# Optimization experiments

Measured on AMD Instinct MI355X. Metric: run time of the kernel, lower is better.

## Reference

```python
import jax, jax.numpy as jnp
import numpy as np

NUM_HEADS = 12


def setup_inputs() -> dict:
    key = jax.random.key(0)
    ks = jax.random.split(key, 6)
    C = 768
    hd = C // NUM_HEADS  # 64
    H = W = 32
    x = jax.random.normal(ks[0], (4, H, W, C), dtype=jnp.float32)
    # Linear weights stored as (in, out) so y = x @ W (+ b)
    Wqkv = jax.random.normal(ks[1], (C, 3 * C), dtype=jnp.float32) * 0.02
    Wproj = jax.random.normal(ks[2], (C, C), dtype=jnp.float32) * 0.02
    bproj = jax.random.normal(ks[3], (C,), dtype=jnp.float32) * 0.02
    rel_pos_h = jax.random.normal(ks[4], (2 * H - 1, hd), dtype=jnp.float32) * 0.02
    rel_pos_w = jax.random.normal(ks[5], (2 * W - 1, hd), dtype=jnp.float32) * 0.02
    return {"x": x, "Wqkv": Wqkv, "Wproj": Wproj, "bproj": bproj,
            "rel_pos_h": rel_pos_h, "rel_pos_w": rel_pos_w}


def _get_rel_pos(size: int, rel_pos: jnp.ndarray) -> jnp.ndarray:
    # q_size == k_size == size; table already has 2*size-1 entries -> no interpolation
    coords = jnp.arange(size)[:, None] - jnp.arange(size)[None, :] + (size - 1)
    return rel_pos[coords]  # (size, size, head_dim)


def reference(x, Wqkv, Wproj, bproj, rel_pos_h, rel_pos_w):
    B, H, W, C = x.shape
    hn = NUM_HEADS
    hd = C // hn
    scale = hd ** (-0.5)
    S = H * W

    qkv = x @ Wqkv                                   # (B,H,W,3C)
    qkv = qkv.reshape(B, S, 3, hn, hd)
    qkv = jnp.transpose(qkv, (2, 0, 3, 1, 4)).reshape(3, B * hn, S, hd)
    q, k, v = qkv[0], qkv[1], qkv[2]                 # each (B*hn, S, hd)

    # decomposed relative position bias
    Rh = _get_rel_pos(H, rel_pos_h)                  # (H,H,hd)
    Rw = _get_rel_pos(W, rel_pos_w)                  # (W,W,hd)
    r_q = q.reshape(B * hn, H, W, hd)
    rel_h = jnp.einsum('bhwc,hkc->bhwk', r_q, Rh)    # (B*hn,H,W,H)
    rel_w = jnp.einsum('bhwc,wkc->bhwk', r_q, Rw)    # (B*hn,H,W,W)
    bias = rel_h[..., :, None] + rel_w[..., None, :] # (B*hn,H,W,H,W)
    bias = bias.reshape(B * hn, S, S)

    scores = scale * jnp.einsum('bqc,bkc->bqk', q, k) + bias
    attn = jax.nn.softmax(scores, axis=-1)
    out = jnp.einsum('bqk,bkc->bqc', attn, v)        # (B*hn,S,hd)

    out = out.reshape(B, hn, H, W, hd)
    out = jnp.transpose(out, (0, 2, 3, 1, 4)).reshape(B, H, W, C)
    return out @ Wproj + bproj
```

## Files before the change

### kernel.cpp

```cpp
#include <hip/hip_runtime.h>
#include <stddef.h>

typedef __bf16 bf16x8 __attribute__((ext_vector_type(8)));
typedef __bf16 bf16x4 __attribute__((ext_vector_type(4)));
typedef float  f32x4  __attribute__((ext_vector_type(4)));

#define MFMA16(a, b, c) __builtin_amdgcn_mfma_f32_16x16x32_bf16((a), (b), (c), 0, 0, 0)

__device__ __forceinline__ void gload_lds16(const void* gsrc, void* ldst) {
    __builtin_amdgcn_global_load_lds(
        (__attribute__((address_space(1))) void*)gsrc,
        (__attribute__((address_space(3))) void*)ldst,
        16, 0, 0);
}

__global__ void prep_kernel(const float* __restrict__ x, __bf16* __restrict__ xbf,
                            const float* __restrict__ Wqkv, __bf16* __restrict__ WqkvT,
                            const float* __restrict__ Wproj, __bf16* __restrict__ WprojT) {
    __shared__ float tile[32][33];
    const int bx = blockIdx.x, tid = threadIdx.x;
    if (bx < 3072) {
        int i = bx * 256 + tid;
        float4 v = ((const float4*)x)[i];
        bf16x4 o = {(__bf16)v.x, (__bf16)v.y, (__bf16)v.z, (__bf16)v.w};
        ((bf16x4*)xbf)[i] = o;
        return;
    }
    const float* in; __bf16* out; int R, C, c0, r0;
    if (bx < 4800) { int bb = bx - 3072; in = Wqkv;  out = WqkvT;  R = 768; C = 2304;
                     c0 = (bb % 72) * 32; r0 = (bb / 72) * 32; }
    else           { int bb = bx - 4800; in = Wproj; out = WprojT; R = 768; C = 768;
                     c0 = (bb % 24) * 32; r0 = (bb / 24) * 32; }
    const int tx = tid & 31, ty = tid >> 5;
#pragma unroll
    for (int i = 0; i < 32; i += 8)
        tile[ty + i][tx] = in[(size_t)(r0 + ty + i) * C + c0 + tx];
    __syncthreads();
#pragma unroll
    for (int i = 0; i < 32; i += 8)
        out[(size_t)(c0 + ty + i) * R + r0 + tx] = (__bf16)tile[tx][ty + i];
}

__device__ __forceinline__ void gemm_core_bk64(
    const __bf16* __restrict__ A, const __bf16* __restrict__ Bt, int K,
    int m0, int n0, __bf16* aT, __bf16* bT, f32x4 acc[4][4]) {
    const int tid  = threadIdx.x;
    const int wid  = tid >> 6, lane = tid & 63;
    const int quad = lane >> 4, l16 = lane & 15;
    const int wm = (wid >> 1) * 64, wn = (wid & 1) * 64;
    const int r_in = lane >> 3;
    const int cswz = ((lane & 7) ^ r_in) * 8;
    const __bf16* gA = A  + (size_t)(m0 + wid * 8 + r_in) * K + cswz;
    const __bf16* gB = Bt + (size_t)(n0 + wid * 8 + r_in) * K + cswz;
    const int sA = (l16 & 7);
    for (int k0 = 0; k0 < K; k0 += 64) {
        __syncthreads();
#pragma unroll
        for (int j = 0; j < 4; j++) {
            gload_lds16(gA + (size_t)(j * 32) * K + k0, aT + (j * 32 + wid * 8) * 64);
            gload_lds16(gB + (size_t)(j * 32) * K + k0, bT + (j * 32 + wid * 8) * 64);
        }
        __syncthreads();
#pragma unroll
        for (int kh = 0; kh < 2; kh++) {
            bf16x8 af[4], bfr[4];
#pragma unroll
            for (int t = 0; t < 4; t++) {
                const int slot = ((kh * 4 + quad) ^ sA) << 3;
                af[t]  = *(const bf16x8*)(aT + (wm + t * 16 + l16) * 64 + slot);
                bfr[t] = *(const bf16x8*)(bT + (wn + t * 16 + l16) * 64 + slot);
            }
#pragma unroll
            for (int rt = 0; rt < 4; rt++)
#pragma unroll
                for (int ct = 0; ct < 4; ct++)
                    acc[rt][ct] = MFMA16(af[rt], bfr[ct], acc[rt][ct]);
        }
    }
}

__global__ __launch_bounds__(256, 3)
void gemm_qkv_kernel(const __bf16* __restrict__ A, const __bf16* __restrict__ Bt,
                     __bf16* __restrict__ qb, __bf16* __restrict__ kb,
                     __bf16* __restrict__ vtb) {
    __shared__ __bf16 aT[8192], bT[8192];
    f32x4 acc[4][4];
#pragma unroll
    for (int i = 0; i < 4; i++)
#pragma unroll
        for (int j = 0; j < 4; j++) { f32x4 z = {0.f, 0.f, 0.f, 0.f}; acc[i][j] = z; }
    const int m0 = blockIdx.x * 128, n0 = blockIdx.y * 128;
    gemm_core_bk64(A, Bt, 768, m0, n0, aT, bT, acc);
    const int tid = threadIdx.x, wid = tid >> 6, lane = tid & 63;
    const int quad = lane >> 4, l16 = lane & 15;
    const int wm = (wid >> 1) * 64, wn = (wid & 1) * 64;
#pragma unroll
    for (int rt = 0; rt < 4; rt++)
#pragma unroll
        for (int ct = 0; ct < 4; ct++) {
            const int ng = n0 + wn + ct * 16 + l16;
            const int which = ng / 768;
            const int rem = ng - which * 768;
            const int hh = rem >> 6, d = rem & 63;
#pragma unroll
            for (int r = 0; r < 4; r++) {
                const int mg = m0 + wm + rt * 16 + quad * 4 + r;
                const int b = mg >> 10, s = mg & 1023;
                const int bh = b * 12 + hh;
                __bf16 bv = (__bf16)acc[rt][ct][r];
                if (which == 0)      qb[((size_t)bh * 1024 + s) * 64 + d] = bv;
                else if (which == 1) kb[((size_t)bh * 1024 + s) * 64 + d] = bv;
                else                 vtb[((size_t)bh * 64 + d) * 1024 + s] = bv;
            }
        }
}

__global__ __launch_bounds__(256, 3)
void gemm_proj_kernel(const __bf16* __restrict__ A, const __bf16* __restrict__ Bt,
                      const float* __restrict__ bias, float* __restrict__ out) {
    __shared__ __bf16 aT[8192], bT[8192];
    f32x4 acc[4][4];
#pragma unroll
    for (int i = 0; i < 4; i++)
#pragma unroll
        for (int j = 0; j < 4; j++) { f32x4 z = {0.f, 0.f, 0.f, 0.f}; acc[i][j] = z; }
    const int m0 = blockIdx.x * 128, n0 = blockIdx.y * 128;
    gemm_core_bk64(A, Bt, 768, m0, n0, aT, bT, acc);
    const int tid = threadIdx.x, wid = tid >> 6, lane = tid & 63;
    const int quad = lane >> 4, l16 = lane & 15;
    const int wm = (wid >> 1) * 64, wn = (wid & 1) * 64;
#pragma unroll
    for (int rt = 0; rt < 4; rt++)
#pragma unroll
        for (int ct = 0; ct < 4; ct++) {
            const int ng = n0 + wn + ct * 16 + l16;
            const float bb = bias[ng];
#pragma unroll
            for (int r = 0; r < 4; r++) {
                const int mg = m0 + wm + rt * 16 + quad * 4 + r;
                out[(size_t)mg * 768 + ng] = acc[rt][ct][r] + bb;
            }
        }
}

__global__ __launch_bounds__(128, 2)
void attn_kernel(const __bf16* __restrict__ q, const __bf16* __restrict__ kk,
                 const __bf16* __restrict__ vt, const float* __restrict__ rph,
                 const float* __restrict__ rpw, __bf16* __restrict__ aout) {
    __shared__ __bf16 kv[2][8192];
    __shared__ __bf16 pbuf[2][32 * 72];
    __shared__ float  relh[64][33];
    const int tid = threadIdx.x, wid = tid >> 6, lane = tid & 63;
    const int quad = lane >> 4, l16 = lane & 15;
    const int bh = blockIdx.x, qt = blockIdx.y;
    const int b = bh / 12, hh = bh - b * 12;
    const int q0 = qt * 64;
    const int w0 = wid * 32;
    const int h = qt * 2 + wid;

    bf16x8 aq[2][2];
#pragma unroll
    for (int rt = 0; rt < 2; rt++) {
        const __bf16* qp = q + ((size_t)bh * 1024 + q0 + w0 + rt * 16 + l16) * 64;
        aq[rt][0] = *(const bf16x8*)(qp + quad * 8);
        aq[rt][1] = *(const bf16x8*)(qp + 32 + quad * 8);
    }

    float* Dw = ((float*)kv) + wid * 2048;
#pragma unroll
    for (int ct = 0; ct < 4; ct++) {
        int j = ct * 16 + l16; if (j > 62) j = 62;
        const float* tb = rpw + (size_t)j * 64;
        float4 t0 = *(const float4*)(tb + quad * 8);
        float4 t1 = *(const float4*)(tb + quad * 8 + 4);
        float4 t2 = *(const float4*)(tb + 32 + quad * 8);
        float4 t3 = *(const float4*)(tb + 32 + quad * 8 + 4);
        bf16x8 b0 = {(__bf16)t0.x, (__bf16)t0.y, (__bf16)t0.z, (__bf16)t0.w,
                     (__bf16)t1.x, (__bf16)t1.y, (__bf16)t1.z, (__bf16)t1.w};
        bf16x8 b1 = {(__bf16)t2.x, (__bf16)t2.y, (__bf16)t2.z, (__bf16)t2.w,
                     (__bf16)t3.x, (__bf16)t3.y, (__bf16)t3.z, (__bf16)t3.w};
#pragma unroll
        for (int rt = 0; rt < 2; rt++) {
            f32x4 z = {0.f, 0.f, 0.f, 0.f};
            z = MFMA16(aq[rt][0], b0, z);
            z = MFMA16(aq[rt][1], b1, z);
#pragma unroll
            for (int i = 0; i < 4; i++)
                Dw[(rt * 16 + quad * 4 + i) * 64 + ct * 16 + l16] = z[i];
        }
    }
#pragma unroll
    for (int ct = 0; ct < 2; ct++) {
        const int tr = h - (ct * 16 + l16) + 31;
        const float* tb = rph + (size_t)tr * 64;
        float4 t0 = *(const float4*)(tb + quad * 8);
        float4 t1 = *(const float4*)(tb + quad * 8 + 4);
        float4 t2 = *(const float4*)(tb + 32 + quad * 8);
        float4 t3 = *(const float4*)(tb + 32 + quad * 8 + 4);
        bf16x8 b0 = {(__bf16)t0.x, (__bf16)t0.y, (__bf16)t0.z, (__bf16)t0.w,
                     (__bf16)t1.x, (__bf16)t1.y, (__bf16)t1.z, (__bf16)t1.w};
        bf16x8 b1 = {(__bf16)t2.x, (__bf16)t2.y, (__bf16)t2.z, (__bf16)t2.w,
                     (__bf16)t3.x, (__bf16)t3.y, (__bf16)t3.z, (__bf16)t3.w};
#pragma unroll
        for (int rt = 0; rt < 2; rt++) {
            f32x4 z = {0.f, 0.f, 0.f, 0.f};
            z = MFMA16(aq[rt][0], b0, z);
            z = MFMA16(aq[rt][1], b1, z);
#pragma unroll
            for (int i = 0; i < 4; i++)
                relh[w0 + rt * 16 + quad * 4 + i][ct * 16 + l16] = z[i];
        }
    }
    float bw[2][2][4];
#pragma unroll
    for (int rt = 0; rt < 2; rt++)
#pragma unroll
        for (int r = 0; r < 4; r++) {
            const int row = rt * 16 + quad * 4 + r;
            bw[rt][0][r] = Dw[row * 64 + row - l16 + 31];
            bw[rt][1][r] = Dw[row * 64 + row + 15 - l16];
        }
    __syncthreads();

    float l_run[2][4];
    f32x4 o_acc[2][4];
#pragma unroll
    for (int rt = 0; rt < 2; rt++)
#pragma unroll
        for (int r = 0; r < 4; r++) l_run[rt][r] = 0.f;
#pragma unroll
    for (int rt = 0; rt < 2; rt++)
#pragma unroll
        for (int t = 0; t < 4; t++) { f32x4 z = {0.f, 0.f, 0.f, 0.f}; o_acc[rt][t] = z; }

    const __bf16* kg0 = kk + (size_t)bh * 65536;
    const __bf16* vg0 = vt + (size_t)bh * 65536;
    const int cbase = wid * 4;
    const int srow = lane >> 3;
    const int scol = ((lane & 7) ^ srow) * 8;
    const int swz0 = ((quad ^ (l16 & 7)) << 3);
    const int swz1 = (((quad | 4) ^ (l16 & 7)) << 3);
    __bf16* pw = pbuf[wid];

    auto stage = [&](int buf, int kt) {
        const __bf16* kg = kg0 + kt * 4096;
        const __bf16* vg = vg0 + kt * 64;
        __bf16* kb_ = &kv[buf][0];
        __bf16* vb_ = &kv[buf][4096];
#pragma unroll
        for (int j = 0; j < 4; j++) {
            const int c = cbase + j;
            gload_lds16(kg + (c * 8 + srow) * 64 + scol, kb_ + c * 512);
            gload_lds16(vg + (size_t)(c * 8 + srow) * 1024 + scol, vb_ + c * 512);
        }
    };

    stage(0, 0);
    for (int kt = 0; kt < 16; kt++) {
        const int cur = kt & 1;
        __syncthreads();
        if (kt < 15) stage(1 - cur, kt + 1);
        const __bf16* kbuf = &kv[cur][0];
        const __bf16* vbuf = &kv[cur][4096];

        bf16x8 bk[4][2];
#pragma unroll
        for (int ct = 0; ct < 4; ct++) {
            const int key = ct * 16 + l16;
            bk[ct][0] = *(const bf16x8*)(kbuf + key * 64 + swz0);
            bk[ct][1] = *(const bf16x8*)(kbuf + key * 64 + swz1);
        }

#pragma unroll
        for (int rt = 0; rt < 2; rt++) {
            f32x4 sacc[4];
#pragma unroll
            for (int ct = 0; ct < 4; ct++) {
                f32x4 z = {0.f, 0.f, 0.f, 0.f};
                z = MFMA16(aq[rt][0], bk[ct][0], z);
                z = MFMA16(aq[rt][1], bk[ct][1], z);
                sacc[ct] = z;
            }
            float bh0[4], bh1[4];
#pragma unroll
            for (int r = 0; r < 4; r++) {
                bh0[r] = relh[w0 + rt * 16 + quad * 4 + r][kt * 2];
                bh1[r] = relh[w0 + rt * 16 + quad * 4 + r][kt * 2 + 1];
            }
#pragma unroll
            for (int ct = 0; ct < 4; ct++)
#pragma unroll
                for (int r = 0; r < 4; r++) {
                    float sv = fmaf(sacc[ct][r], 0.125f,
                                    (ct < 2 ? bh0[r] : bh1[r]) +
                                    ((ct & 1) ? bw[rt][1][r] : bw[rt][0][r]));
                    float p = __expf(sv);
                    l_run[rt][r] += p;
                    pw[(rt * 16 + quad * 4 + r) * 72 + ct * 16 + l16] = (__bf16)p;
                }
        }

#pragma unroll
        for (int nt = 0; nt < 4; nt++) {
            const int d = nt * 16 + l16;
            bf16x8 bv0 = *(const bf16x8*)(vbuf + d * 64 + swz0);
            bf16x8 bv1 = *(const bf16x8*)(vbuf + d * 64 + swz1);
#pragma unroll
            for (int rt = 0; rt < 2; rt++) {
                bf16x8 ap0 = *(const bf16x8*)(pw + (rt * 16 + l16) * 72 + quad * 8);
                bf16x8 ap1 = *(const bf16x8*)(pw + (rt * 16 + l16) * 72 + 32 + quad * 8);
                o_acc[rt][nt] = MFMA16(ap0, bv0, o_acc[rt][nt]);
                o_acc[rt][nt] = MFMA16(ap1, bv1, o_acc[rt][nt]);
            }
        }
    }

#pragma unroll
    for (int rt = 0; rt < 2; rt++)
#pragma unroll
        for (int r = 0; r < 4; r++) {
            float s = l_run[rt][r];
            s += __shfl_xor(s, 1);
            s += __shfl_xor(s, 2);
            s += __shfl_xor(s, 4);
            s += __shfl_xor(s, 8);
            l_run[rt][r] = 1.f / s;
        }
#pragma unroll
    for (int rt = 0; rt < 2; rt++) {
        const int srow_o = q0 + w0 + rt * 16 + quad * 4;
#pragma unroll
        for (int nt = 0; nt < 4; nt++)
#pragma unroll
            for (int r = 0; r < 4; r++) {
                float v = o_acc[rt][nt][r] * l_run[rt][r];
                aout[((size_t)b * 1024 + srow_o + r) * 768 + hh * 64 + nt * 16 + l16] = (__bf16)v;
            }
    }
}

extern "C" void kernel_launch(void* const* d_in, const int* in_sizes, int n_in,
                              void* d_out, int out_size, void* d_ws, size_t ws_size,
                              hipStream_t stream) {
    const float* x     = (const float*)d_in[0];
    const float* Wqkv  = (const float*)d_in[1];
    const float* Wproj = (const float*)d_in[2];
    const float* bproj = (const float*)d_in[3];
    const float* rph   = (const float*)d_in[4];
    const float* rpw   = (const float*)d_in[5];
    float* out = (float*)d_out;
    char* ws = (char*)d_ws;

    __bf16* xbf    = (__bf16*)(ws);
    __bf16* WqkvT  = (__bf16*)(ws + 6291456);
    __bf16* WprojT = (__bf16*)(ws + 9830400);
    __bf16* qb     = (__bf16*)(ws + 11010048);
    __bf16* kb     = (__bf16*)(ws + 17301504);
    __bf16* vtb    = (__bf16*)(ws + 23592960);
    __bf16* aob    = (__bf16*)(ws + 29884416);

    prep_kernel<<<dim3(5376), dim3(256), 0, stream>>>(x, xbf, Wqkv, WqkvT, Wproj, WprojT);
    gemm_qkv_kernel<<<dim3(32, 18), dim3(256), 0, stream>>>(xbf, WqkvT, qb, kb, vtb);
    attn_kernel<<<dim3(48, 16), dim3(128), 0, stream>>>(qb, kb, vtb, rph, rpw, aob);
    gemm_proj_kernel<<<dim3(32, 6), dim3(256), 0, stream>>>(aob, WprojT, bproj, out);
}
```

Before: 154.4 us.

## Split attention query tile across four waves of 16 rows each

```diff
diff --git a/kernel.cpp b/kernel.cpp
--- a/kernel.cpp
+++ b/kernel.cpp
@@ -143,30 +143,26 @@
         }
 }
 
-__global__ __launch_bounds__(128, 2)
+__global__ __launch_bounds__(256, 3)
 void attn_kernel(const __bf16* __restrict__ q, const __bf16* __restrict__ kk,
                  const __bf16* __restrict__ vt, const float* __restrict__ rph,
                  const float* __restrict__ rpw, __bf16* __restrict__ aout) {
     __shared__ __bf16 kv[2][8192];
-    __shared__ __bf16 pbuf[2][32 * 72];
+    __shared__ __bf16 pbuf[4][16 * 72];
     __shared__ float  relh[64][33];
     const int tid = threadIdx.x, wid = tid >> 6, lane = tid & 63;
     const int quad = lane >> 4, l16 = lane & 15;
     const int bh = blockIdx.x, qt = blockIdx.y;
     const int b = bh / 12, hh = bh - b * 12;
     const int q0 = qt * 64;
-    const int w0 = wid * 32;
-    const int h = qt * 2 + wid;
-
-    bf16x8 aq[2][2];
-#pragma unroll
-    for (int rt = 0; rt < 2; rt++) {
-        const __bf16* qp = q + ((size_t)bh * 1024 + q0 + w0 + rt * 16 + l16) * 64;
-        aq[rt][0] = *(const bf16x8*)(qp + quad * 8);
-        aq[rt][1] = *(const bf16x8*)(qp + 32 + quad * 8);
-    }
-
-    float* Dw = ((float*)kv) + wid * 2048;
+    const int w0 = wid * 16;
+    const int h = qt * 2 + (wid >> 1);
+
+    const __bf16* qp = q + ((size_t)bh * 1024 + q0 + w0 + l16) * 64;
+    bf16x8 aq0 = *(const bf16x8*)(qp + quad * 8);
+    bf16x8 aq1 = *(const bf16x8*)(qp + 32 + quad * 8);
+
+    float* Dw = ((float*)kv) + wid * 1024;
 #pragma unroll
     for (int ct = 0; ct < 4; ct++) {
         int j = ct * 16 + l16; if (j > 62) j = 62;
@@ -179,15 +175,12 @@
                      (__bf16)t1.x, (__bf16)t1.y, (__bf16)t1.z, (__bf16)t1.w};
         bf16x8 b1 = {(__bf16)t2.x, (__bf16)t2.y, (__bf16)t2.z, (__bf16)t2.w,
                      (__bf16)t3.x, (__bf16)t3.y, (__bf16)t3.z, (__bf16)t3.w};
-#pragma unroll
-        for (int rt = 0; rt < 2; rt++) {
-            f32x4 z = {0.f, 0.f, 0.f, 0.f};
-            z = MFMA16(aq[rt][0], b0, z);
-            z = MFMA16(aq[rt][1], b1, z);
-#pragma unroll
-            for (int i = 0; i < 4; i++)
-                Dw[(rt * 16 + quad * 4 + i) * 64 + ct * 16 + l16] = z[i];
-        }
+        f32x4 z = {0.f, 0.f, 0.f, 0.f};
+        z = MFMA16(aq0, b0, z);
+        z = MFMA16(aq1, b1, z);
+#pragma unroll
+        for (int i = 0; i < 4; i++)
+            Dw[(quad * 4 + i) * 64 + ct * 16 + l16] = z[i];
     }
 #pragma unroll
     for (int ct = 0; ct < 2; ct++) {
@@ -201,41 +194,33 @@
                      (__bf16)t1.x, (__bf16)t1.y, (__bf16)t1.z, (__bf16)t1.w};
         bf16x8 b1 = {(__bf16)t2.x, (__bf16)t2.y, (__bf16)t2.z, (__bf16)t2.w,
                      (__bf16)t3.x, (__bf16)t3.y, (__bf16)t3.z, (__bf16)t3.w};
-#pragma unroll
-        for (int rt = 0; rt < 2; rt++) {
-            f32x4 z = {0.f, 0.f, 0.f, 0.f};
-            z = MFMA16(aq[rt][0], b0, z);
-            z = MFMA16(aq[rt][1], b1, z);
-#pragma unroll
-            for (int i = 0; i < 4; i++)
-                relh[w0 + rt * 16 + quad * 4 + i][ct * 16 + l16] = z[i];
-        }
-    }
-    float bw[2][2][4];
-#pragma unroll
-    for (int rt = 0; rt < 2; rt++)
-#pragma unroll
-        for (int r = 0; r < 4; r++) {
-            const int row = rt * 16 + quad * 4 + r;
-            bw[rt][0][r] = Dw[row * 64 + row - l16 + 31];
-            bw[rt][1][r] = Dw[row * 64 + row + 15 - l16];
-        }
+        f32x4 z = {0.f, 0.f, 0.f, 0.f};
+        z = MFMA16(aq0, b0, z);
+        z = MFMA16(aq1, b1, z);
+#pragma unroll
+        for (int i = 0; i < 4; i++)
+            relh[w0 + quad * 4 + i][ct * 16 + l16] = z[i];
+    }
+    float bw[2][4];
+#pragma unroll
+    for (int r = 0; r < 4; r++) {
+        const int rl = quad * 4 + r;
+        const int w = (wid & 1) * 16 + rl;
+        bw[0][r] = Dw[rl * 64 + w - l16 + 31];
+        bw[1][r] = Dw[rl * 64 + w + 15 - l16];
+    }
     __syncthreads();
 
-    float l_run[2][4];
-    f32x4 o_acc[2][4];
-#pragma unroll
-    for (int rt = 0; rt < 2; rt++)
-#pragma unroll
-        for (int r = 0; r < 4; r++) l_run[rt][r] = 0.f;
-#pragma unroll
-    for (int rt = 0; rt < 2; rt++)
-#pragma unroll
-        for (int t = 0; t < 4; t++) { f32x4 z = {0.f, 0.f, 0.f, 0.f}; o_acc[rt][t] = z; }
+    float l_run[4];
+    f32x4 o_acc[4];
+#pragma unroll
+    for (int r = 0; r < 4; r++) l_run[r] = 0.f;
+#pragma unroll
+    for (int t = 0; t < 4; t++) { f32x4 z = {0.f, 0.f, 0.f, 0.f}; o_acc[t] = z; }
 
     const __bf16* kg0 = kk + (size_t)bh * 65536;
     const __bf16* vg0 = vt + (size_t)bh * 65536;
-    const int cbase = wid * 4;
+    const int cbase = wid * 2;
     const int srow = lane >> 3;
     const int scol = ((lane & 7) ^ srow) * 8;
     const int swz0 = ((quad ^ (l16 & 7)) << 3);
@@ -248,7 +233,7 @@
         __bf16* kb_ = &kv[buf][0];
         __bf16* vb_ = &kv[buf][4096];
 #pragma unroll
-        for (int j = 0; j < 4; j++) {
+        for (int j = 0; j < 2; j++) {
             const int c = cbase + j;
             gload_lds16(kg + (c * 8 + srow) * 64 + scol, kb_ + c * 512);
             gload_lds16(vg + (size_t)(c * 8 + srow) * 1024 + scol, vb_ + c * 512);
@@ -271,72 +256,60 @@
             bk[ct][1] = *(const bf16x8*)(kbuf + key * 64 + swz1);
         }
 
-#pragma unroll
-        for (int rt = 0; rt < 2; rt++) {
-            f32x4 sacc[4];
-#pragma unroll
-            for (int ct = 0; ct < 4; ct++) {
-                f32x4 z = {0.f, 0.f, 0.f, 0.f};
-                z = MFMA16(aq[rt][0], bk[ct][0], z);
-                z = MFMA16(aq[rt][1], bk[ct][1], z);
-                sacc[ct] = z;
+        f32x4 sacc[4];
+#pragma unroll
+        for (int ct = 0; ct < 4; ct++) {
+            f32x4 z = {0.f, 0.f, 0.f, 0.f};
+            z = MFMA16(aq0, bk[ct][0], z);
+            z = MFMA16(aq1, bk[ct][1], z);
+            sacc[ct] = z;
+        }
+        float bh0[4], bh1[4];
+#pragma unroll
+        for (int r = 0; r < 4; r++) {
+            bh0[r] = relh[w0 + quad * 4 + r][kt * 2];
+            bh1[r] = relh[w0 + quad * 4 + r][kt * 2 + 1];
+        }
+#pragma unroll
+        for (int ct = 0; ct < 4; ct++)
+#pragma unroll
+            for (int r = 0; r < 4; r++) {
+                float sv = fmaf(sacc[ct][r], 0.125f,
+                                (ct < 2 ? bh0[r] : bh1[r]) + ((ct & 1) ? bw[1][r] : bw[0][r]));
+                float p = __expf(sv);
+                l_run[r] += p;
+                pw[(quad * 4 + r) * 72 + ct * 16 + l16] = (__bf16)p;
             }
-            float bh0[4], bh1[4];
-#pragma unroll
-            for (int r = 0; r < 4; r++) {
-                bh0[r] = relh[w0 + rt * 16 + quad * 4 + r][kt * 2];
-                bh1[r] = relh[w0 + rt * 16 + quad * 4 + r][kt * 2 + 1];
-            }
-#pragma unroll
-            for (int ct = 0; ct < 4; ct++)
-#pragma unroll
-                for (int r = 0; r < 4; r++) {
-                    float sv = fmaf(sacc[ct][r], 0.125f,
-                                    (ct < 2 ? bh0[r] : bh1[r]) +
-                                    ((ct & 1) ? bw[rt][1][r] : bw[rt][0][r]));
-                    float p = __expf(sv);
-                    l_run[rt][r] += p;
-                    pw[(rt * 16 + quad * 4 + r) * 72 + ct * 16 + l16] = (__bf16)p;
-                }
-        }
-
+
+        bf16x8 ap0 = *(const bf16x8*)(pw + l16 * 72 + quad * 8);
+        bf16x8 ap1 = *(const bf16x8*)(pw + l16 * 72 + 32 + quad * 8);
 #pragma unroll
         for (int nt = 0; nt < 4; nt++) {
             const int d = nt * 16 + l16;
             bf16x8 bv0 = *(const bf16x8*)(vbuf + d * 64 + swz0);
             bf16x8 bv1 = *(const bf16x8*)(vbuf + d * 64 + swz1);
-#pragma unroll
-            for (int rt = 0; rt < 2; rt++) {
-                bf16x8 ap0 = *(const bf16x8*)(pw + (rt * 16 + l16) * 72 + quad * 8);
-                bf16x8 ap1 = *(const bf16x8*)(pw + (rt * 16 + l16) * 72 + 32 + quad * 8);
-                o_acc[rt][nt] = MFMA16(ap0, bv0, o_acc[rt][nt]);
-                o_acc[rt][nt] = MFMA16(ap1, bv1, o_acc[rt][nt]);
-            }
-        }
-    }
-
-#pragma unroll
-    for (int rt = 0; rt < 2; rt++)
+            o_acc[nt] = MFMA16(ap0, bv0, o_acc[nt]);
+            o_acc[nt] = MFMA16(ap1, bv1, o_acc[nt]);
+        }
+    }
+
+#pragma unroll
+    for (int r = 0; r < 4; r++) {
+        float s = l_run[r];
+        s += __shfl_xor(s, 1);
+        s += __shfl_xor(s, 2);
+        s += __shfl_xor(s, 4);
+        s += __shfl_xor(s, 8);
+        l_run[r] = 1.f / s;
+    }
+    const int srow_o = q0 + w0 + quad * 4;
+#pragma unroll
+    for (int nt = 0; nt < 4; nt++)
 #pragma unroll
         for (int r = 0; r < 4; r++) {
-            float s = l_run[rt][r];
-            s += __shfl_xor(s, 1);
-            s += __shfl_xor(s, 2);
-            s += __shfl_xor(s, 4);
-            s += __shfl_xor(s, 8);
-            l_run[rt][r] = 1.f / s;
-        }
-#pragma unroll
-    for (int rt = 0; rt < 2; rt++) {
-        const int srow_o = q0 + w0 + rt * 16 + quad * 4;
-#pragma unroll
-        for (int nt = 0; nt < 4; nt++)
-#pragma unroll
-            for (int r = 0; r < 4; r++) {
-                float v = o_acc[rt][nt][r] * l_run[rt][r];
-                aout[((size_t)b * 1024 + srow_o + r) * 768 + hh * 64 + nt * 16 + l16] = (__bf16)v;
-            }
-    }
+            float v = o_acc[nt][r] * l_run[r];
+            aout[((size_t)b * 1024 + srow_o + r) * 768 + hh * 64 + nt * 16 + l16] = (__bf16)v;
+        }
 }
 
 extern "C" void kernel_launch(void* const* d_in, const int* in_sizes, int n_in,
@@ -361,6 +334,6 @@
 
     prep_kernel<<<dim3(5376), dim3(256), 0, stream>>>(x, xbf, Wqkv, WqkvT, Wproj, WprojT);
     gemm_qkv_kernel<<<dim3(32, 18), dim3(256), 0, stream>>>(xbf, WqkvT, qb, kb, vtb);
-    attn_kernel<<<dim3(48, 16), dim3(128), 0, stream>>>(qb, kb, vtb, rph, rpw, aob);
+    attn_kernel<<<dim3(48, 16), dim3(256), 0, stream>>>(qb, kb, vtb, rph, rpw, aob);
     gemm_proj_kernel<<<dim3(32, 6), dim3(256), 0, stream>>>(aob, WprojT, bproj, out);
 }
```

Measured after the change: 155.1 us. Within noise of the previous version (+0.5%).
